# Performance work log

Hardware: AMD Instinct MI355X
Metric: run time of the kernel (lower is better)

## Reference

```python
import jax, jax.numpy as jnp
import numpy as np

B, NV, NC, D, E = 16, 8192, 4096, 128, 49152


def _gru_cell(x, h, w_ih, w_hh, b_ih, b_hh):
    """torch.nn.GRUCell math; gate order r, z, n; weights are (3D, D)."""
    gi = x @ w_ih.T + b_ih
    gh = h @ w_hh.T + b_hh
    ir, iz, inn = jnp.split(gi, 3, axis=-1)
    hr, hz, hn = jnp.split(gh, 3, axis=-1)
    r = jax.nn.sigmoid(ir + hr)
    z = jax.nn.sigmoid(iz + hz)
    n = jnp.tanh(inn + r * hn)
    return (1.0 - z) * n + z * h


def _msg_net(x, w1, b1, w2, b2):
    # Linear -> exact GELU -> Linear (torch nn.GELU default is erf-based)
    return jax.nn.gelu(x @ w1.T + b1, approximate=False) @ w2.T + b2


def _spmm(feats, src_idx, dst_idx, n_out):
    """Binary sparse-matrix @ dense: gather rows at src_idx, segment-sum to dst_idx.
    feats: (B, N_src, D) -> (B, n_out, D). Equivalent to torch.sparse.mm(H, feats[i])."""
    gathered = feats[:, src_idx, :]  # (B, E, D)
    return jax.vmap(lambda g: jax.ops.segment_sum(g, dst_idx, num_segments=n_out))(gathered)


def setup_inputs() -> dict:
    key = jax.random.key(0)
    ks = jax.random.split(key, 20)
    s = 0.05
    inp = {
        "v_feats": jax.random.normal(ks[0], (B, NV, D), jnp.float32),
        "c_feats": jax.random.normal(ks[1], (B, NC, D), jnp.float32),
        "edge_chk": jax.random.randint(ks[2], (E,), 0, NC, jnp.int32),
        "edge_var": jax.random.randint(ks[3], (E,), 0, NV, jnp.int32),
        # msg_net: Linear(D,D) -> GELU -> Linear(D,D)
        "msg_w1": jax.random.normal(ks[4], (D, D), jnp.float32) * s,
        "msg_b1": jnp.zeros((D,), jnp.float32),
        "msg_w2": jax.random.normal(ks[5], (D, D), jnp.float32) * s,
        "msg_b2": jnp.zeros((D,), jnp.float32),
        # var_update GRUCell(D, D)
        "var_w_ih": jax.random.normal(ks[6], (3 * D, D), jnp.float32) * s,
        "var_w_hh": jax.random.normal(ks[7], (3 * D, D), jnp.float32) * s,
        "var_b_ih": jnp.zeros((3 * D,), jnp.float32),
        "var_b_hh": jnp.zeros((3 * D,), jnp.float32),
        # chk_update GRUCell(D, D)
        "chk_w_ih": jax.random.normal(ks[8], (3 * D, D), jnp.float32) * s,
        "chk_w_hh": jax.random.normal(ks[9], (3 * D, D), jnp.float32) * s,
        "chk_b_ih": jnp.zeros((3 * D,), jnp.float32),
        "chk_b_hh": jnp.zeros((3 * D,), jnp.float32),
    }
    return inp


def reference(v_feats, c_feats, edge_chk, edge_var,
              msg_w1, msg_b1, msg_w2, msg_b2,
              var_w_ih, var_w_hh, var_b_ih, var_b_hh,
              chk_w_ih, chk_w_hh, chk_b_ih, chk_b_hh):
    b, nv, d = v_feats.shape
    nc = c_feats.shape[1]
    # variable -> check: H @ v_feats (H is binary, rows=checks, cols=vars)
    v_to_c = _spmm(v_feats, edge_var, edge_chk, nc)        # (B, NC, D)
    v_to_c = _msg_net(v_to_c, msg_w1, msg_b1, msg_w2, msg_b2)
    c_new = _gru_cell(v_to_c.reshape(-1, d), c_feats.reshape(-1, d),
                      chk_w_ih, chk_w_hh, chk_b_ih, chk_b_hh).reshape(b, nc, d)
    # check -> variable: H^T @ c_new
    c_to_v = _spmm(c_new, edge_chk, edge_var, nv)          # (B, NV, D)
    c_to_v = _msg_net(c_to_v, msg_w1, msg_b1, msg_w2, msg_b2)
    v_new = _gru_cell(c_to_v.reshape(-1, d), v_feats.reshape(-1, d),
                      var_w_ih, var_w_hh, var_b_ih, var_b_hh).reshape(b, nv, d)
    return (v_new, c_new)
```

## Files before the change

kernel.cpp:

```cpp
#include <hip/hip_runtime.h>

using u16 = unsigned short;
using u32 = unsigned int;
using u64 = unsigned long long;
typedef short short8 __attribute__((ext_vector_type(8)));
typedef unsigned short ushort8 __attribute__((ext_vector_type(8)));
typedef float f32x4 __attribute__((ext_vector_type(4)));

#define GB  16
#define GNV 8192
#define GNC 4096
#define GD  128
#define GE  49152

#define MFMA __builtin_amdgcn_mfma_f32_16x16x32_bf16


__device__ __forceinline__ u16 f2bf(float f){
    u32 u = __builtin_bit_cast(u32, f);
    u32 r = (u >> 16) & 1u;
    u += 0x7fffu + r;
    return (u16)(u >> 16);
}

__device__ __forceinline__ float bf2f(u16 x){
    return __builtin_bit_cast(float, (u32)x << 16);
}

__device__ __forceinline__ u32 cvtpk(float lo, float hi){
    u32 r;
    asm("v_cvt_pk_bf16_f32 %0, %1, %2" : "=v"(r) : "v"(lo), "v"(hi));
    return r;
}

__device__ __forceinline__ u64 pack4(float a, float b, float c, float d){
    return (u64)cvtpk(a, b) | ((u64)cvtpk(c, d) << 32);
}

__device__ __forceinline__ float sigmoidf_(float x){
    return __fdividef(1.f, 1.f + __expf(-x));
}

__device__ __forceinline__ float tanhf_fast(float x){
    float xc = fminf(15.f, fmaxf(-15.f, x));
    float t  = __expf(2.f * xc);
    return __fdividef(t - 1.f, t + 1.f);
}

__device__ __forceinline__ char* swzp(const void* base, int row, int bc){
    return (char*)base + row * 256 + (bc ^ ((row & 7) << 4));
}

__device__ __forceinline__ short8 ldfrag(const u16* tile, int row, int lane, int ks){
    int bc = ks * 64 + ((lane >> 4) << 4);
    return *(const short8*)swzp(tile, row, bc);
}


__global__ void k_hist(const int* __restrict__ ec, const int* __restrict__ ev,
                       int* cc, int* cv){
    int e = blockIdx.x * 256 + threadIdx.x;
    if (e < GE){ atomicAdd(&cc[ec[e]], 1); atomicAdd(&cv[ev[e]], 1); }
}

__global__ __launch_bounds__(1024) void k_scan(const int* __restrict__ cnt, int* off, int n){
    __shared__ int part[1024];
    int tid = threadIdx.x;
    int chunk = n >> 10;
    int base = tid * chunk;
    int s = 0;
    for (int i = 0; i < chunk; ++i) s += cnt[base + i];
    part[tid] = s;
    __syncthreads();
    #pragma unroll
    for (int ofs = 1; ofs < 1024; ofs <<= 1){
        int v = (tid >= ofs) ? part[tid - ofs] : 0;
        __syncthreads();
        part[tid] += v;
        __syncthreads();
    }
    if (tid == 1023) off[n] = part[1023];
    int run = part[tid] - s;
    for (int i = 0; i < chunk; ++i){ off[base + i] = run; run += cnt[base + i]; }
}

__global__ void k_fill(const int* __restrict__ ec, const int* __restrict__ ev,
                       int* cur_c, int* lst_c, int* cur_v, int* lst_v){
    int e = blockIdx.x * 256 + threadIdx.x;
    if (e < GE){
        int c = ec[e], v = ev[e];
        lst_c[atomicAdd(&cur_c[c], 1)] = v;
        lst_v[atomicAdd(&cur_v[v], 1)] = c;
    }
}

__global__ void k_sort(const int* __restrict__ off, int* lst, int n){
    int i = blockIdx.x * 256 + threadIdx.x;
    if (i >= n) return;
    int s = off[i], e = off[i + 1];
    for (int a = s + 1; a < e; ++a){
        int v = lst[a]; int b = a - 1;
        while (b >= s && lst[b] > v){ lst[b + 1] = lst[b]; --b; }
        lst[b + 1] = v;
    }
}

__global__ void k_cvt(const float* __restrict__ s, u16* d, int n){
    int i = blockIdx.x * 256 + threadIdx.x;
    if (i < n) d[i] = f2bf(s[i]);
}


__global__ __launch_bounds__(256) void k_tr(const float* __restrict__ src,
                                            u16* __restrict__ dstT, int n){
    const int node = blockIdx.x, t = threadIdx.x;
    const int b = t >> 4, d0 = (t & 15) * 8;
    const float4* s = (const float4*)(src + ((size_t)b * n + node) * GD + d0);
    float4 v0 = s[0], v1 = s[1];
    u64* p = (u64*)(dstT + (size_t)node * 2048 + t * 8);
    p[0] = pack4(v0.x, v0.y, v0.z, v0.w);
    p[1] = pack4(v1.x, v1.y, v1.z, v1.w);
}


__global__ __launch_bounds__(256) void k_spmm(const u16* __restrict__ srcT,
                                              const int* __restrict__ off,
                                              const int* __restrict__ lst,
                                              u16* __restrict__ dst, int ndst){
    const int node = blockIdx.x, t = threadIdx.x;
    const int b = t >> 4, d0 = (t & 15) * 8;
    float acc[8];
    #pragma unroll
    for (int i = 0; i < 8; ++i) acc[i] = 0.f;
    const int s = off[node], e = off[node + 1];
    const u16* base = srcT + t * 8;
    for (int a = s; a < e; ++a){
        ushort8 v = *(const ushort8*)(base + (size_t)lst[a] * 2048);
        #pragma unroll
        for (int i = 0; i < 8; ++i) acc[i] += bf2f(v[i]);
    }
    u64* p = (u64*)(dst + ((size_t)b * ndst + node) * GD + d0);
    p[0] = pack4(acc[0], acc[1], acc[2], acc[3]);
    p[1] = pack4(acc[4], acc[5], acc[6], acc[7]);
}


__global__ __launch_bounds__(512, 2) void k_msg(u16* __restrict__ X,
                                                const u16* __restrict__ W1, const float* __restrict__ b1,
                                                const u16* __restrict__ W2, const float* __restrict__ b2,
                                                int ntiles){
    __shared__ __align__(16) u16 Xs[2][64 * 128];
    __shared__ __align__(16) u16 Gs[64 * 128];
    const int tid = threadIdx.x, lane = tid & 63, w = tid >> 6;
    const int l15 = lane & 15, rg = lane >> 4;
    const int j = w * 16 + l15;

    short8 w1f[4], w2f[4];
    #pragma unroll
    for (int ks = 0; ks < 4; ++ks){
        w1f[ks] = *(const short8*)(W1 + (size_t)j * 128 + ks * 32 + rg * 8);
        w2f[ks] = *(const short8*)(W2 + (size_t)j * 128 + ks * 32 + rg * 8);
    }
    const float bb1 = b1[j], bb2 = b2[j];

    const int nk = ntiles / gridDim.x;
    u64 xr[4];
    auto issue = [&](int tt){
        const u64* xs = (const u64*)(X + (size_t)tt * 64 * 128);
        #pragma unroll
        for (int i = 0; i < 4; ++i) xr[i] = xs[tid + i * 512];
    };

    issue(blockIdx.x);
    for (int k = 0; k < nk; ++k){
        const int buf = k & 1;
        #pragma unroll
        for (int i = 0; i < 4; ++i){
            int idx = tid + i * 512;
            *(u64*)swzp(Xs[buf], idx >> 5, (idx & 31) << 3) = xr[i];
        }
        __syncthreads();
        if (k + 1 < nk) issue(blockIdx.x + (k + 1) * gridDim.x);

        #pragma unroll
        for (int sub = 0; sub < 4; ++sub){
            const u16* xt = Xs[buf] + sub * 16 * 128;
            f32x4 acc = {0, 0, 0, 0};
            #pragma unroll
            for (int ks = 0; ks < 4; ++ks)
                acc = MFMA(ldfrag(xt, l15, lane, ks), w1f[ks], acc, 0, 0, 0);
            #pragma unroll
            for (int i = 0; i < 4; ++i){
                float v = acc[i] + bb1;
                float g = 0.5f * v * (1.f + erff(v * 0.70710678f));
                *(u16*)swzp(Gs, sub * 16 + rg * 4 + i, j * 2) = f2bf(g);
            }
        }
        __syncthreads();

        const size_t row0 = (size_t)(blockIdx.x + (size_t)k * gridDim.x) * 64;
        #pragma unroll
        for (int sub = 0; sub < 4; ++sub){
            const u16* gt = Gs + sub * 16 * 128;
            f32x4 acc = {0, 0, 0, 0};
            #pragma unroll
            for (int ks = 0; ks < 4; ++ks)
                acc = MFMA(ldfrag(gt, l15, lane, ks), w2f[ks], acc, 0, 0, 0);
            #pragma unroll
            for (int i = 0; i < 4; ++i)
                X[(row0 + sub * 16 + rg * 4 + i) * GD + j] = f2bf(acc[i] + bb2);
        }
    }
}


__global__ __launch_bounds__(512, 2) void k_gru(const u16* __restrict__ Xb, const float* __restrict__ Hf,
                                                const u16* __restrict__ Wih, const float* __restrict__ bih,
                                                const u16* __restrict__ Whh, const float* __restrict__ bhh,
                                                float* __restrict__ Out, u16* __restrict__ OutT,
                                                int logN, int ntiles){
    __shared__ __align__(16) u16 Xs[2][64 * 128];
    __shared__ __align__(16) u16 Hs[2][64 * 128];
    const int tid = threadIdx.x, lane = tid & 63, w = tid >> 6;
    const int l15 = lane & 15, rg = lane >> 4;
    const int j = w * 16 + l15;
    const int nmask = (1 << logN) - 1;

    short8 wf[6][4];
    #pragma unroll
    for (int g = 0; g < 3; ++g){
        #pragma unroll
        for (int ks = 0; ks < 4; ++ks){
            wf[g][ks]     = *(const short8*)(Wih + (size_t)(g * 128 + j) * 128 + ks * 32 + rg * 8);
            wf[g + 3][ks] = *(const short8*)(Whh + (size_t)(g * 128 + j) * 128 + ks * 32 + rg * 8);
        }
    }
    const float bir = bih[j]       + bhh[j];
    const float biz = bih[128 + j] + bhh[128 + j];
    const float bin = bih[256 + j];
    const float bhn = bhh[256 + j];

    const int nk = ntiles / gridDim.x;
    const int crow = (tid * 2) >> 4, cc = ((tid * 2) & 15) << 4;

    ushort8 xrA[2], xrB[2]; float4 hrA[4], hrB[4];

    auto issue = [&](ushort8* xr, float4* hr, int t){
        const ushort8* xs = (const ushort8*)(Xb + (size_t)t * 8192) + tid * 2;
        const float4*  hs = (const float4*) (Hf + (size_t)t * 8192) + tid * 4;
        xr[0] = xs[0]; xr[1] = xs[1];
        #pragma unroll
        for (int i = 0; i < 4; ++i) hr[i] = hs[i];
    };

    auto commit = [&](const ushort8* xr, const float4* hr, int buf){
        *(ushort8*)swzp(Xs[buf], crow, cc)      = xr[0];
        *(ushort8*)swzp(Xs[buf], crow, cc + 16) = xr[1];
        union { u32 u[4]; ushort8 v; } q0, q1;
        q0.u[0] = cvtpk(hr[0].x, hr[0].y); q0.u[1] = cvtpk(hr[0].z, hr[0].w);
        q0.u[2] = cvtpk(hr[1].x, hr[1].y); q0.u[3] = cvtpk(hr[1].z, hr[1].w);
        q1.u[0] = cvtpk(hr[2].x, hr[2].y); q1.u[1] = cvtpk(hr[2].z, hr[2].w);
        q1.u[2] = cvtpk(hr[3].x, hr[3].y); q1.u[3] = cvtpk(hr[3].z, hr[3].w);
        *(ushort8*)swzp(Hs[buf], crow, cc)      = q0.v;
        *(ushort8*)swzp(Hs[buf], crow, cc + 16) = q1.v;
    };

    auto compute = [&](int t, int buf){
        const float* hg = Hf  + (size_t)t * 8192;
        float*       og = Out + (size_t)t * 8192;
        #pragma unroll
        for (int sub = 0; sub < 4; ++sub){
            const u16* xt = Xs[buf] + sub * 2048;
            const u16* ht = Hs[buf] + sub * 2048;
            float h0[4];
            #pragma unroll
            for (int i = 0; i < 4; ++i) h0[i] = hg[(sub * 16 + rg * 4 + i) * 128 + j];
            f32x4 ar = {0,0,0,0}, az = {0,0,0,0}, an = {0,0,0,0}, hn = {0,0,0,0};
            #pragma unroll
            for (int ks = 0; ks < 4; ++ks){
                short8 a = ldfrag(xt, l15, lane, ks);
                short8 h = ldfrag(ht, l15, lane, ks);
                ar = MFMA(a, wf[0][ks], ar, 0, 0, 0);
                az = MFMA(a, wf[1][ks], az, 0, 0, 0);
                an = MFMA(a, wf[2][ks], an, 0, 0, 0);
                ar = MFMA(h, wf[3][ks], ar, 0, 0, 0);
                az = MFMA(h, wf[4][ks], az, 0, 0, 0);
                hn = MFMA(h, wf[5][ks], hn, 0, 0, 0);
            }
            #pragma unroll
            for (int i = 0; i < 4; ++i){
                int r = sub * 16 + rg * 4 + i;
                float rr = sigmoidf_(ar[i] + bir);
                float zz = sigmoidf_(az[i] + biz);
                float nn = tanhf_fast(an[i] + bin + rr * (hn[i] + bhn));
                float val = (1.f - zz) * nn + zz * h0[i];
                og[r * 128 + j] = val;
                if (OutT){
                    int grow = t * 64 + r;
                    int bidx = grow >> logN, node = grow & nmask;
                    OutT[(((size_t)node << 4) + bidx) * GD + j] = f2bf(val);
                }
            }
        }
    };

    issue(xrA, hrA, blockIdx.x);
    issue(xrB, hrB, blockIdx.x + gridDim.x);
    for (int k = 0; k < nk; k += 2){
        const int t0 = blockIdx.x + k * gridDim.x;
        commit(xrA, hrA, 0);
        __syncthreads();
        if (k + 2 < nk) issue(xrA, hrA, t0 + 2 * gridDim.x);
        compute(t0, 0);

        const int t1 = t0 + gridDim.x;
        commit(xrB, hrB, 1);
        __syncthreads();
        if (k + 3 < nk) issue(xrB, hrB, t1 + 2 * gridDim.x);
        compute(t1, 1);
    }
}


extern "C" void kernel_launch(void* const* d_in, const int* in_sizes, int n_in,
                              void* d_out, int out_size, void* d_ws, size_t ws_size,
                              hipStream_t stream){
    const float* v_feats  = (const float*)d_in[0];
    const float* c_feats  = (const float*)d_in[1];
    const int*   edge_chk = (const int*)d_in[2];
    const int*   edge_var = (const int*)d_in[3];
    const float* msg_w1   = (const float*)d_in[4];
    const float* msg_b1   = (const float*)d_in[5];
    const float* msg_w2   = (const float*)d_in[6];
    const float* msg_b2   = (const float*)d_in[7];
    const float* var_w_ih = (const float*)d_in[8];
    const float* var_w_hh = (const float*)d_in[9];
    const float* var_b_ih = (const float*)d_in[10];
    const float* var_b_hh = (const float*)d_in[11];
    const float* chk_w_ih = (const float*)d_in[12];
    const float* chk_w_hh = (const float*)d_in[13];
    const float* chk_b_ih = (const float*)d_in[14];
    const float* chk_b_hh = (const float*)d_in[15];

    float* out_v = (float*)d_out;
    float* out_c = out_v + (size_t)GB * GNV * GD;

    char* p = (char*)d_ws;
    auto take = [&](size_t bytes) -> void* {
        void* r = (void*)p; p += (bytes + 255) & ~(size_t)255; return r;
    };
    int* cnt_c = (int*)take(GNC * 4);
    int* cnt_v = (int*)take(GNV * 4);
    int* off_c = (int*)take((GNC + 1) * 4);
    int* off_v = (int*)take((GNV + 1) * 4);
    int* cur_c = (int*)take(GNC * 4);
    int* cur_v = (int*)take(GNV * 4);
    int* lst_c = (int*)take(GE * 4);
    int* lst_v = (int*)take(GE * 4);
    u16* w1b  = (u16*)take((size_t)GD * GD * 2);
    u16* w2b  = (u16*)take((size_t)GD * GD * 2);
    u16* cihb = (u16*)take((size_t)3 * GD * GD * 2);
    u16* chhb = (u16*)take((size_t)3 * GD * GD * 2);
    u16* vihb = (u16*)take((size_t)3 * GD * GD * 2);
    u16* vhhb = (u16*)take((size_t)3 * GD * GD * 2);
    u16* mc = (u16*)take((size_t)GB * GNC * GD * 2);
    u16* mv = (u16*)take((size_t)GB * GNV * GD * 2);
    u16* vT = (u16*)take((size_t)GNV * GB * GD * 2);
    u16* cT = (u16*)take((size_t)GNC * GB * GD * 2);

    hipMemsetAsync(cnt_c, 0, GNC * 4, stream);
    hipMemsetAsync(cnt_v, 0, GNV * 4, stream);
    k_hist<<<(GE + 255) / 256, 256, 0, stream>>>(edge_chk, edge_var, cnt_c, cnt_v);
    k_scan<<<1, 1024, 0, stream>>>(cnt_c, off_c, GNC);
    k_scan<<<1, 1024, 0, stream>>>(cnt_v, off_v, GNV);
    hipMemcpyAsync(cur_c, off_c, GNC * 4, hipMemcpyDeviceToDevice, stream);
    hipMemcpyAsync(cur_v, off_v, GNV * 4, hipMemcpyDeviceToDevice, stream);
    k_fill<<<(GE + 255) / 256, 256, 0, stream>>>(edge_chk, edge_var, cur_c, lst_c, cur_v, lst_v);
    k_sort<<<(GNC + 255) / 256, 256, 0, stream>>>(off_c, lst_c, GNC);
    k_sort<<<(GNV + 255) / 256, 256, 0, stream>>>(off_v, lst_v, GNV);

    k_cvt<<<(GD * GD + 255) / 256, 256, 0, stream>>>(msg_w1, w1b, GD * GD);
    k_cvt<<<(GD * GD + 255) / 256, 256, 0, stream>>>(msg_w2, w2b, GD * GD);
    k_cvt<<<(3 * GD * GD + 255) / 256, 256, 0, stream>>>(chk_w_ih, cihb, 3 * GD * GD);
    k_cvt<<<(3 * GD * GD + 255) / 256, 256, 0, stream>>>(chk_w_hh, chhb, 3 * GD * GD);
    k_cvt<<<(3 * GD * GD + 255) / 256, 256, 0, stream>>>(var_w_ih, vihb, 3 * GD * GD);
    k_cvt<<<(3 * GD * GD + 255) / 256, 256, 0, stream>>>(var_w_hh, vhhb, 3 * GD * GD);
    k_tr<<<GNV, 256, 0, stream>>>(v_feats, vT, GNV);

    k_spmm<<<GNC, 256, 0, stream>>>(vT, off_c, lst_c, mc, GNC);
    k_msg<<<256, 512, 0, stream>>>(mc, w1b, msg_b1, w2b, msg_b2, (GB * GNC) / 64);
    k_gru<<<256, 512, 0, stream>>>(mc, c_feats, cihb, chk_b_ih, chhb, chk_b_hh,
                                   out_c, cT, 12, (GB * GNC) / 64);
    k_spmm<<<GNV, 256, 0, stream>>>(cT, off_v, lst_v, mv, GNV);
    k_msg<<<256, 512, 0, stream>>>(mv, w1b, msg_b1, w2b, msg_b2, (GB * GNV) / 64);
    k_gru<<<256, 512, 0, stream>>>(mv, v_feats, vihb, var_b_ih, vhhb, var_b_hh,
                                   out_v, (u16*)nullptr, 13, (GB * GNV) / 64);
}
```

Before: 341.1 us.

## Feed GRU hidden state from bf16 transposed copies and double GRU/msg grid

The GRU kernel now reads the hidden state from node-major bf16 transposed buffers (the existing vT, plus a new cfT made by transposing c_feats) instead of fp32 row-major features. This halves hidden-state load bytes and drops the in-kernel fp32-to-bf16 packing. The h0 used in the final blend comes from the bf16 shared tile rather than a separate fp32 global read. Launch grids for k_msg and k_gru grow from 256 to 512 blocks. The costs are an extra transpose kernel for c_feats and lower precision for the z*h term, which now uses a bf16-rounded h.

```diff
diff --git a/kernel.cpp b/kernel.cpp
--- a/kernel.cpp
+++ b/kernel.cpp
@@ -214,7 +214,7 @@
 }
 
 
-__global__ __launch_bounds__(512, 2) void k_gru(const u16* __restrict__ Xb, const float* __restrict__ Hf,
+__global__ __launch_bounds__(512, 2) void k_gru(const u16* __restrict__ Xb, const u16* __restrict__ HT,
                                                 const u16* __restrict__ Wih, const float* __restrict__ bih,
                                                 const u16* __restrict__ Whh, const float* __restrict__ bhh,
                                                 float* __restrict__ Out, u16* __restrict__ OutT,
@@ -241,40 +241,32 @@
     const float bhn = bhh[256 + j];
 
     const int nk = ntiles / gridDim.x;
-    const int crow = (tid * 2) >> 4, cc = ((tid * 2) & 15) << 4;
-
-    ushort8 xrA[2], xrB[2]; float4 hrA[4], hrB[4];
-
-    auto issue = [&](ushort8* xr, float4* hr, int t){
+    const int crow = tid >> 3, cc = (tid & 7) * 32;
+
+    ushort8 xrA[2], xrB[2], hrA[2], hrB[2];
+
+    auto issue = [&](ushort8* xr, ushort8* hr, int t){
         const ushort8* xs = (const ushort8*)(Xb + (size_t)t * 8192) + tid * 2;
-        const float4*  hs = (const float4*) (Hf + (size_t)t * 8192) + tid * 4;
         xr[0] = xs[0]; xr[1] = xs[1];
-        #pragma unroll
-        for (int i = 0; i < 4; ++i) hr[i] = hs[i];
-    };
-
-    auto commit = [&](const ushort8* xr, const float4* hr, int buf){
+        int grow = t * 64 + crow;
+        int node = grow & nmask, b = grow >> logN;
+        const ushort8* hs = (const ushort8*)(HT + (((size_t)node << 4) + b) * GD + (tid & 7) * 16);
+        hr[0] = hs[0]; hr[1] = hs[1];
+    };
+
+    auto commit = [&](const ushort8* xr, const ushort8* hr, int buf){
         *(ushort8*)swzp(Xs[buf], crow, cc)      = xr[0];
         *(ushort8*)swzp(Xs[buf], crow, cc + 16) = xr[1];
-        union { u32 u[4]; ushort8 v; } q0, q1;
-        q0.u[0] = cvtpk(hr[0].x, hr[0].y); q0.u[1] = cvtpk(hr[0].z, hr[0].w);
-        q0.u[2] = cvtpk(hr[1].x, hr[1].y); q0.u[3] = cvtpk(hr[1].z, hr[1].w);
-        q1.u[0] = cvtpk(hr[2].x, hr[2].y); q1.u[1] = cvtpk(hr[2].z, hr[2].w);
-        q1.u[2] = cvtpk(hr[3].x, hr[3].y); q1.u[3] = cvtpk(hr[3].z, hr[3].w);
-        *(ushort8*)swzp(Hs[buf], crow, cc)      = q0.v;
-        *(ushort8*)swzp(Hs[buf], crow, cc + 16) = q1.v;
+        *(ushort8*)swzp(Hs[buf], crow, cc)      = hr[0];
+        *(ushort8*)swzp(Hs[buf], crow, cc + 16) = hr[1];
     };
 
     auto compute = [&](int t, int buf){
-        const float* hg = Hf  + (size_t)t * 8192;
-        float*       og = Out + (size_t)t * 8192;
+        float* og = Out + (size_t)t * 8192;
         #pragma unroll
         for (int sub = 0; sub < 4; ++sub){
             const u16* xt = Xs[buf] + sub * 2048;
             const u16* ht = Hs[buf] + sub * 2048;
-            float h0[4];
-            #pragma unroll
-            for (int i = 0; i < 4; ++i) h0[i] = hg[(sub * 16 + rg * 4 + i) * 128 + j];
             f32x4 ar = {0,0,0,0}, az = {0,0,0,0}, an = {0,0,0,0}, hn = {0,0,0,0};
             #pragma unroll
             for (int ks = 0; ks < 4; ++ks){
@@ -290,10 +282,12 @@
             #pragma unroll
             for (int i = 0; i < 4; ++i){
                 int r = sub * 16 + rg * 4 + i;
+                int rl = rg * 4 + i;
+                float h0 = bf2f(*(const u16*)swzp(ht, rl, j * 2));
                 float rr = sigmoidf_(ar[i] + bir);
                 float zz = sigmoidf_(az[i] + biz);
                 float nn = tanhf_fast(an[i] + bin + rr * (hn[i] + bhn));
-                float val = (1.f - zz) * nn + zz * h0[i];
+                float val = (1.f - zz) * nn + zz * h0;
                 og[r * 128 + j] = val;
                 if (OutT){
                     int grow = t * 64 + r;
@@ -367,6 +361,7 @@
     u16* mv = (u16*)take((size_t)GB * GNV * GD * 2);
     u16* vT = (u16*)take((size_t)GNV * GB * GD * 2);
     u16* cT = (u16*)take((size_t)GNC * GB * GD * 2);
+    u16* cfT= (u16*)take((size_t)GNC * GB * GD * 2);
 
     hipMemsetAsync(cnt_c, 0, GNC * 4, stream);
     hipMemsetAsync(cnt_v, 0, GNV * 4, stream);
@@ -386,13 +381,14 @@
     k_cvt<<<(3 * GD * GD + 255) / 256, 256, 0, stream>>>(var_w_ih, vihb, 3 * GD * GD);
     k_cvt<<<(3 * GD * GD + 255) / 256, 256, 0, stream>>>(var_w_hh, vhhb, 3 * GD * GD);
     k_tr<<<GNV, 256, 0, stream>>>(v_feats, vT, GNV);
+    k_tr<<<GNC, 256, 0, stream>>>(c_feats, cfT, GNC);
 
     k_spmm<<<GNC, 256, 0, stream>>>(vT, off_c, lst_c, mc, GNC);
-    k_msg<<<256, 512, 0, stream>>>(mc, w1b, msg_b1, w2b, msg_b2, (GB * GNC) / 64);
-    k_gru<<<256, 512, 0, stream>>>(mc, c_feats, cihb, chk_b_ih, chhb, chk_b_hh,
+    k_msg<<<512, 512, 0, stream>>>(mc, w1b, msg_b1, w2b, msg_b2, (GB * GNC) / 64);
+    k_gru<<<512, 512, 0, stream>>>(mc, cfT, cihb, chk_b_ih, chhb, chk_b_hh,
                                    out_c, cT, 12, (GB * GNC) / 64);
     k_spmm<<<GNV, 256, 0, stream>>>(cT, off_v, lst_v, mv, GNV);
-    k_msg<<<256, 512, 0, stream>>>(mv, w1b, msg_b1, w2b, msg_b2, (GB * GNV) / 64);
-    k_gru<<<256, 512, 0, stream>>>(mv, v_feats, vihb, var_b_ih, vhhb, var_b_hh,
+    k_msg<<<512, 512, 0, stream>>>(mv, w1b, msg_b1, w2b, msg_b2, (GB * GNV) / 64);
+    k_gru<<<512, 512, 0, stream>>>(mv, vT, vihb, var_b_ih, vhhb, var_b_hh,
                                    out_v, (u16*)nullptr, 13, (GB * GNV) / 64);
 }
```

Measured after the change: 355.2 us. 1.04x slower.
